# Performance work log

Hardware: AMD Instinct MI355X
Metric: run time of the kernel (lower is better)

## Reference

```python
import jax, jax.numpy as jnp
import numpy as np

EPS = 0.1
MAX_ITER = 100
THRESH = 0.1


def setup_inputs() -> dict:
    key = jax.random.key(0)
    k1, k2, k3, k4 = jax.random.split(key, 4)
    N, P1, P2, D = 4, 1024, 1024, 16
    x = jax.random.normal(k1, (N, P1, D), dtype=jnp.float32)
    y = jax.random.normal(k2, (N, P2, D), dtype=jnp.float32)
    wx = jax.random.uniform(k3, (N, P1), dtype=jnp.float32)
    wy = jax.random.uniform(k4, (N, P2), dtype=jnp.float32)
    # normalize to probability weights (typical usage for empirical measures)
    wx = wx / jnp.sum(wx, axis=-1, keepdims=True)
    wy = wy / jnp.sum(wy, axis=-1, keepdims=True)
    return {"x": x, "y": y, "wx": wx, "wy": wy}


def _cost_matrix(x, y):
    # |x_i - y_j|^1 summed over feature dim -> [N, P1, P2]
    return jnp.sum(jnp.abs(x[:, :, None, :] - y[:, None, :, :]), axis=-1)


def reference(x, y, wx, wy):
    C = _cost_matrix(x, y)                     # [N, P1, P2]
    mu, nu = wx, wy                            # [N, P1], [N, P2]
    log_mu = jnp.log(mu + 1e-8)
    log_nu = jnp.log(nu + 1e-8)

    def M(u, v):
        # (-C_ij + u_i + v_j) / eps
        return (-C + u[:, :, None] + v[:, None, :]) / EPS

    def step(carry, _):
        u, v, done = carry
        u_new = EPS * (log_mu - jax.nn.logsumexp(M(u, v), axis=-1)) + u
        v_new = EPS * (log_nu - jax.nn.logsumexp(M(u_new, v), axis=-2)) + v
        err = jnp.mean(jnp.sum(jnp.abs(u_new - u), axis=-1))
        # emulate torch's early break: freeze u,v once converged
        u_out = jnp.where(done, u, u_new)
        v_out = jnp.where(done, v, v_new)
        done = done | (err < THRESH)
        return (u_out, v_out, done), None

    u0 = jnp.zeros_like(mu)
    v0 = jnp.zeros_like(nu)
    (u, v, _), _ = jax.lax.scan(step, (u0, v0, jnp.array(False)), None, length=MAX_ITER)

    pi = jnp.exp(M(u, v))                      # transport plan [N, P1, P2]
    cost = jnp.sum(pi * C, axis=(-2, -1))      # [N]  (reduction='none')
    return cost, pi, C
```

## Files before the change

### kernel.cpp

```cpp
#include <hip/hip_runtime.h>

static constexpr int   NB      = 4;
static constexpr int   PP      = 1024;
static constexpr int   DD      = 16;
static constexpr float EPSV    = 0.1f;
static constexpr float KE      = 14.42695041f;
static constexpr float KL      = 0.0693147181f;
static constexpr int   MAXIT   = 100;
static constexpr float THRESHV = 0.1f;

static constexpr int NBLK = 256;
static constexpr int NTHR = 512;
static constexpr unsigned DONEG = 1000000u;

__device__ __forceinline__ float fexp2(float v) { return __builtin_amdgcn_exp2f(v); }
__device__ __forceinline__ float flog2(float v) { return __builtin_amdgcn_logf(v); }

static constexpr int    ERR_F_OFF     = 4352;
static constexpr size_t WS_ZERO_BYTES = 4352 * 4;
static constexpr size_t ERR_BYTES    = 512 * 4;

static constexpr int VSNAP_OFF = 131072;

__device__ __forceinline__ float aload(const float* p) {
    return __hip_atomic_load(p, __ATOMIC_RELAXED, __HIP_MEMORY_SCOPE_AGENT);
}
__device__ __forceinline__ void astore(float* p, float v) {
    __hip_atomic_store(p, v, __ATOMIC_RELAXED, __HIP_MEMORY_SCOPE_AGENT);
}
__device__ __forceinline__ unsigned aloadu(const unsigned* p) {
    return __hip_atomic_load(p, __ATOMIC_RELAXED, __HIP_MEMORY_SCOPE_AGENT);
}
__device__ __forceinline__ void astoreu(unsigned* p, unsigned v) {
    __hip_atomic_store(p, v, __ATOMIC_RELAXED, __HIP_MEMORY_SCOPE_AGENT);
}
__device__ __forceinline__ float2 aload2(const float* p) {
    unsigned long long v = __hip_atomic_load((const unsigned long long*)p,
                                             __ATOMIC_RELAXED, __HIP_MEMORY_SCOPE_AGENT);
    union { unsigned long long u; float f[2]; } c; c.u = v;
    return make_float2(c.f[0], c.f[1]);
}
__device__ __forceinline__ void astore2(float* p, float a, float b) {
    union { unsigned long long u; float f[2]; } c; c.f[0] = a; c.f[1] = b;
    __hip_atomic_store((unsigned long long*)p, c.u,
                       __ATOMIC_RELAXED, __HIP_MEMORY_SCOPE_AGENT);
}

__device__ __forceinline__ void gbar_group(unsigned* ws32, int n, int g, unsigned gen) {
    __syncthreads();
    if (threadIdx.x < 64) {
        if (threadIdx.x == 0) astoreu(ws32 + (n * 64 + g) * 16, gen);
        const unsigned* sp = ws32 + (n * 64 + threadIdx.x) * 16;
        while (__ballot(aloadu(sp) >= gen) != ~0ull)
            __builtin_amdgcn_s_sleep(1);
    }
    __syncthreads();
}

__global__ __launch_bounds__(NTHR, 2)
void sinkhorn_kernel(const float* __restrict__ x, const float* __restrict__ y,
                     const float* __restrict__ wx, const float* __restrict__ wy,
                     float* __restrict__ out, float* __restrict__ ws)
{
    __shared__ float rt[16 * PP];
    __shared__ float sbuf[PP];
    __shared__ float cred[8];
    __shared__ int   Ts;

    unsigned* ws32  = (unsigned*)ws;
    unsigned* Tslot = ws32 + 4096;
    unsigned* exitf = ws32 + 4104;
    float*    ews   = ws + ERR_F_OFF;

    float* out_cost = out;
    float* out_pi   = out + NB;
    float* out_C    = out + NB + (size_t)NB * PP * PP;

    const int b   = blockIdx.x;
    const int n   = b >> 6;
    const int g   = b & 63;
    const int i0  = g * 16;
    const int w   = threadIdx.x >> 6;
    const int l   = threadIdx.x & 63;
    const int tid = threadIdx.x;

    float* sc = out_C + (size_t)n * PP * PP;

    float4 xr[2][4];
    #pragma unroll
    for (int rr = 0; rr < 2; ++rr) {
        const float4* xp = (const float4*)(x + ((size_t)n * PP + (i0 + 2 * w + rr)) * DD);
        #pragma unroll
        for (int q = 0; q < 4; ++q) xr[rr][q] = xp[q];
    }
    #pragma unroll 4
    for (int k = 0; k < 16; ++k) {
        int j = l + 64 * k;
        const float4* yp = (const float4*)(y + ((size_t)n * PP + j) * DD);
        float4 y0 = yp[0], y1 = yp[1], y2 = yp[2], y3 = yp[3];
        #pragma unroll
        for (int rr = 0; rr < 2; ++rr) {
            float c = fabsf(xr[rr][0].x - y0.x) + fabsf(xr[rr][0].y - y0.y)
                    + fabsf(xr[rr][0].z - y0.z) + fabsf(xr[rr][0].w - y0.w)
                    + fabsf(xr[rr][1].x - y1.x) + fabsf(xr[rr][1].y - y1.y)
                    + fabsf(xr[rr][1].z - y1.z) + fabsf(xr[rr][1].w - y1.w)
                    + fabsf(xr[rr][2].x - y2.x) + fabsf(xr[rr][2].y - y2.y)
                    + fabsf(xr[rr][2].z - y2.z) + fabsf(xr[rr][2].w - y2.w)
                    + fabsf(xr[rr][3].x - y3.x) + fabsf(xr[rr][3].y - y3.y)
                    + fabsf(xr[rr][3].z - y3.z) + fabsf(xr[rr][3].w - y3.w);
            rt[(2 * w + rr) * PP + j] = c;
        }
    }

    float4 yc[2][4];
    #pragma unroll
    for (int c = 0; c < 2; ++c) {
        const float4* yp = (const float4*)(y + ((size_t)n * PP + (i0 + 2 * w + c)) * DD);
        #pragma unroll
        for (int q = 0; q < 4; ++q) yc[c][q] = yp[q];
    }
    float2 c2[16];
    #pragma unroll 4
    for (int k = 0; k < 16; ++k) {
        const float4* xp = (const float4*)(x + ((size_t)n * PP + (l + 64 * k)) * DD);
        float4 x0 = xp[0], x1 = xp[1], x2 = xp[2], x3 = xp[3];
        float cc[2];
        #pragma unroll
        for (int c = 0; c < 2; ++c) {
            cc[c] = fabsf(x0.x - yc[c][0].x) + fabsf(x0.y - yc[c][0].y)
                  + fabsf(x0.z - yc[c][0].z) + fabsf(x0.w - yc[c][0].w)
                  + fabsf(x1.x - yc[c][1].x) + fabsf(x1.y - yc[c][1].y)
                  + fabsf(x1.z - yc[c][1].z) + fabsf(x1.w - yc[c][1].w)
                  + fabsf(x2.x - yc[c][2].x) + fabsf(x2.y - yc[c][2].y)
                  + fabsf(x2.z - yc[c][2].z) + fabsf(x2.w - yc[c][2].w)
                  + fabsf(x3.x - yc[c][3].x) + fabsf(x3.y - yc[c][3].y)
                  + fabsf(x3.z - yc[c][3].z) + fabsf(x3.w - yc[c][3].w);
        }
        c2[k] = make_float2(cc[0], cc[1]);
    }

    float lmu[2], lnu[2];
    #pragma unroll
    for (int rr = 0; rr < 2; ++rr) {
        lmu[rr] = __logf(wx[n * PP + i0 + 2 * w + rr] + 1e-8f);
        lnu[rr] = __logf(wy[n * PP + i0 + 2 * w + rr] + 1e-8f);
    }

    float uprev0 = 0.f, uprev1 = 0.f;

    #pragma unroll 1
    for (int t = 0; t < MAXIT; ++t) {
        if (t >= 2) {
            unsigned ef = aloadu(exitf + n);
            if (ef != 0u && t >= (int)ef + 1) break;
        }

        if (t == 0) {
            sbuf[2 * tid] = 0.f; sbuf[2 * tid + 1] = 0.f;
        } else {
            float2 vp = aload2(sc + VSNAP_OFF + (size_t)(t - 1) * PP + 2 * tid);
            sbuf[2 * tid] = vp.x; sbuf[2 * tid + 1] = vp.y;
        }
        __syncthreads();

        {
            float4 tt[2][4];
            float m0 = -3.4e38f, m1 = -3.4e38f;
            #pragma unroll
            for (int k = 0; k < 4; ++k) {
                int j = 256 * k + 4 * l;
                float4 v4 = *(const float4*)&sbuf[j];
                float4 ca = *(const float4*)&rt[(2 * w) * PP + j];
                float4 cb = *(const float4*)&rt[(2 * w + 1) * PP + j];
                tt[0][k] = make_float4(v4.x - ca.x, v4.y - ca.y, v4.z - ca.z, v4.w - ca.w);
                tt[1][k] = make_float4(v4.x - cb.x, v4.y - cb.y, v4.z - cb.z, v4.w - cb.w);
                m0 = fmaxf(m0, fmaxf(fmaxf(tt[0][k].x, tt[0][k].y), fmaxf(tt[0][k].z, tt[0][k].w)));
                m1 = fmaxf(m1, fmaxf(fmaxf(tt[1][k].x, tt[1][k].y), fmaxf(tt[1][k].z, tt[1][k].w)));
            }
            #pragma unroll
            for (int off = 32; off >= 1; off >>= 1) {
                m0 = fmaxf(m0, __shfl_xor(m0, off));
                m1 = fmaxf(m1, __shfl_xor(m1, off));
            }
            float s0 = 0.f, s1 = 0.f;
            #pragma unroll
            for (int k = 0; k < 4; ++k) {
                s0 += fexp2((tt[0][k].x - m0) * KE) + fexp2((tt[0][k].y - m0) * KE)
                    + fexp2((tt[0][k].z - m0) * KE) + fexp2((tt[0][k].w - m0) * KE);
                s1 += fexp2((tt[1][k].x - m1) * KE) + fexp2((tt[1][k].y - m1) * KE)
                    + fexp2((tt[1][k].z - m1) * KE) + fexp2((tt[1][k].w - m1) * KE);
            }
            #pragma unroll
            for (int off = 32; off >= 1; off >>= 1) {
                s0 += __shfl_xor(s0, off);
                s1 += __shfl_xor(s1, off);
            }
            float un0 = EPSV * lmu[0] - (m0 + KL * flog2(s0));
            float un1 = EPSV * lmu[1] - (m1 + KL * flog2(s1));
            if (l == 0) astore2(sc + (size_t)t * PP + i0 + 2 * w, un0, un1);
        }

        gbar_group(ws32, n, g, (unsigned)(2 * t + 1));

        {
            float2 up = aload2(sc + (size_t)t * PP + 2 * tid);
            sbuf[2 * tid] = up.x; sbuf[2 * tid + 1] = up.y;
            float we = fabsf(up.x - uprev0) + fabsf(up.y - uprev1);
            uprev0 = up.x; uprev1 = up.y;
            #pragma unroll
            for (int off = 32; off >= 1; off >>= 1) we += __shfl_xor(we, off);
            if (l == 0) cred[w] = we;
        }
        __syncthreads();

        {
            float tt0[16], tt1[16], m0 = -3.4e38f, m1 = -3.4e38f;
            #pragma unroll
            for (int k = 0; k < 16; ++k) {
                float uu = sbuf[l + 64 * k];
                tt0[k] = uu - c2[k].x;
                tt1[k] = uu - c2[k].y;
                m0 = fmaxf(m0, tt0[k]);
                m1 = fmaxf(m1, tt1[k]);
            }
            #pragma unroll
            for (int off = 32; off >= 1; off >>= 1) {
                m0 = fmaxf(m0, __shfl_xor(m0, off));
                m1 = fmaxf(m1, __shfl_xor(m1, off));
            }
            float s0 = 0.f, s1 = 0.f;
            #pragma unroll
            for (int k = 0; k < 16; ++k) {
                s0 += fexp2((tt0[k] - m0) * KE);
                s1 += fexp2((tt1[k] - m1) * KE);
            }
            #pragma unroll
            for (int off = 32; off >= 1; off >>= 1) {
                s0 += __shfl_xor(s0, off);
                s1 += __shfl_xor(s1, off);
            }
            float vn0 = EPSV * lnu[0] - (m0 + KL * flog2(s0));
            float vn1 = EPSV * lnu[1] - (m1 + KL * flog2(s1));
            if (l == 0)
                astore2(sc + VSNAP_OFF + (size_t)t * PP + i0 + 2 * w, vn0, vn1);
        }
        if (g == 0 && tid == 0) {
            float es = cred[0] + cred[1] + cred[2] + cred[3]
                     + cred[4] + cred[5] + cred[6] + cred[7];
            astore(ews + n * 128 + t, es);
        }

        __syncthreads();
        if (tid < 64) {
            if (tid == 0) astoreu(ws32 + (n * 64 + g) * 16, (unsigned)(2 * t + 2));
            if (g == 0) {
                float s1f = aload(ews + 0 * 128 + tid) + aload(ews + 1 * 128 + tid)
                          + aload(ews + 2 * 128 + tid) + aload(ews + 3 * 128 + tid);
                float s2f = aload(ews + 0 * 128 + 64 + tid) + aload(ews + 1 * 128 + 64 + tid)
                          + aload(ews + 2 * 128 + 64 + tid) + aload(ews + 3 * 128 + 64 + tid);
                unsigned long long bb = __ballot(s1f < THRESHV * (float)NB)
                                      | __ballot(s2f < THRESHV * (float)NB);
                if (bb != 0ull && tid == 0 && aloadu(exitf + n) == 0u)
                    astoreu(exitf + n, (unsigned)(t + 1));
            }
            const unsigned* sp = ws32 + (n * 64 + tid) * 16;
            while (__ballot(aloadu(sp) >= (unsigned)(2 * t + 2)) != ~0ull)
                __builtin_amdgcn_s_sleep(1);
        }
        __syncthreads();
    }

    if (g == 0 && tid == 0) astoreu(ws32 + (n * 64) * 16, DONEG);

    if (b == 0 && tid < 64) {
        for (;;) {
            bool ok = (tid >= 4) || (aloadu(ws32 + tid * 64 * 16) >= DONEG);
            if (__ballot(ok) == ~0ull) break;
            __builtin_amdgcn_s_sleep(2);
        }
        float s1f = aload(ews + 0 * 128 + tid) + aload(ews + 1 * 128 + tid)
                  + aload(ews + 2 * 128 + tid) + aload(ews + 3 * 128 + tid);
        float s2f = aload(ews + 0 * 128 + 64 + tid) + aload(ews + 1 * 128 + 64 + tid)
                  + aload(ews + 2 * 128 + 64 + tid) + aload(ews + 3 * 128 + 64 + tid);
        unsigned long long b1 = __ballot(s1f < THRESHV * (float)NB);
        unsigned long long b2 = __ballot(s2f < THRESHV * (float)NB);
        int T = b1 ? (__ffsll((long long)b1) - 1)
                   : (b2 ? 64 + (__ffsll((long long)b2) - 1) : MAXIT - 1);
        if (tid == 0) astoreu(Tslot, (unsigned)(T + 1));
    }
    if (tid == 0) {
        unsigned tv;
        while ((tv = aloadu(Tslot)) == 0u) __builtin_amdgcn_s_sleep(2);
        Ts = (int)tv - 1;
    }
    __syncthreads();
    const int T = Ts;

    float u_loc[2];
    {
        float2 up = aload2(sc + (size_t)T * PP + i0 + 2 * w);
        u_loc[0] = up.x; u_loc[1] = up.y;
        float2 vp = aload2(sc + VSNAP_OFF + (size_t)T * PP + 2 * tid);
        sbuf[2 * tid] = vp.x; sbuf[2 * tid + 1] = vp.y;
    }
    gbar_group(ws32, n, g, DONEG + 1u);

    float cacc = 0.f;
    #pragma unroll
    for (int rr = 0; rr < 2; ++rr) {
        int r = 2 * w + rr;
        int i = i0 + r;
        float un = u_loc[rr];
        #pragma unroll
        for (int k = 0; k < 4; ++k) {
            int j = 256 * k + 4 * l;
            float4 c4 = *(const float4*)&rt[r * PP + j];
            float4 v4 = *(const float4*)&sbuf[j];
            float4 p4;
            p4.x = fexp2((un + v4.x - c4.x) * KE);
            p4.y = fexp2((un + v4.y - c4.y) * KE);
            p4.z = fexp2((un + v4.z - c4.z) * KE);
            p4.w = fexp2((un + v4.w - c4.w) * KE);
            *(float4*)&out_pi[((size_t)n * PP + i) * PP + j] = p4;
            *(float4*)&out_C [((size_t)n * PP + i) * PP + j] = c4;
            cacc += p4.x * c4.x + p4.y * c4.y + p4.z * c4.z + p4.w * c4.w;
        }
    }
    #pragma unroll
    for (int off = 32; off >= 1; off >>= 1) cacc += __shfl_xor(cacc, off);
    if (l == 0) cred[w] = cacc;
    __syncthreads();
    if (tid == 0) {
        float s = 0.f;
        #pragma unroll
        for (int q = 0; q < 8; ++q) s += cred[q];
        atomicAdd(&out_cost[n], s);
    }
}

extern "C" void kernel_launch(void* const* d_in, const int* in_sizes, int n_in,
                              void* d_out, int out_size, void* d_ws, size_t ws_size,
                              hipStream_t stream) {
    const float* x  = (const float*)d_in[0];
    const float* y  = (const float*)d_in[1];
    const float* wx = (const float*)d_in[2];
    const float* wy = (const float*)d_in[3];
    float* out = (float*)d_out;
    float* ws  = (float*)d_ws;

    (void)hipMemsetAsync(d_ws, 0, WS_ZERO_BYTES, stream);
    (void)hipMemsetAsync((char*)d_ws + WS_ZERO_BYTES, 0x7f, ERR_BYTES, stream);
    (void)hipMemsetAsync(d_out, 0, NB * sizeof(float), stream);

    hipLaunchKernelGGL(sinkhorn_kernel, dim3(NBLK), dim3(NTHR), 0, stream,
                       x, y, wx, wy, out, ws);
}
```

Before: 805.4 us.

## Replace per-half-iteration group barriers with tagged dataflow polling on u/v values

Removes the two group-wide barriers per Sinkhorn iteration. Each u/v value is now stored as a 64-bit word carrying the float and a tag, and consumers spin until the tags are nonzero, which gives fine-grained producer-consumer synchronisation. Early-exit detection moves to group 0, which piggybacks an exit bit on its u tags so all blocks can stop on the same iteration. In exchange, the scratch area inside out_C doubles in size and must be zeroed by an extra large memset before every launch, and polling on individual elements adds memory traffic.

```diff
diff --git a/kernel.cpp b/kernel.cpp
--- a/kernel.cpp
+++ b/kernel.cpp
@@ -11,17 +11,20 @@
 
 static constexpr int NBLK = 256;
 static constexpr int NTHR = 512;
-static constexpr unsigned DONEG = 1000000u;
+static constexpr unsigned DONEG   = 1000000u;
+static constexpr unsigned TAG1    = 1u;
+static constexpr unsigned EXITBIT = 2u;
+
+static constexpr int    ERR_F_OFF     = 4352;
+static constexpr size_t WS_ZERO_BYTES = 4352 * 4;
+static constexpr size_t ERR_BYTES     = 512 * 4;
+
+static constexpr int    VOFF = MAXIT * PP;
+static constexpr size_t TAGB = (size_t)2 * MAXIT * PP * 8;
 
 __device__ __forceinline__ float fexp2(float v) { return __builtin_amdgcn_exp2f(v); }
 __device__ __forceinline__ float flog2(float v) { return __builtin_amdgcn_logf(v); }
 
-static constexpr int    ERR_F_OFF     = 4352;
-static constexpr size_t WS_ZERO_BYTES = 4352 * 4;
-static constexpr size_t ERR_BYTES    = 512 * 4;
-
-static constexpr int VSNAP_OFF = 131072;
-
 __device__ __forceinline__ float aload(const float* p) {
     return __hip_atomic_load(p, __ATOMIC_RELAXED, __HIP_MEMORY_SCOPE_AGENT);
 }
@@ -34,16 +37,24 @@
 __device__ __forceinline__ void astoreu(unsigned* p, unsigned v) {
     __hip_atomic_store(p, v, __ATOMIC_RELAXED, __HIP_MEMORY_SCOPE_AGENT);
 }
-__device__ __forceinline__ float2 aload2(const float* p) {
-    unsigned long long v = __hip_atomic_load((const unsigned long long*)p,
-                                             __ATOMIC_RELAXED, __HIP_MEMORY_SCOPE_AGENT);
-    union { unsigned long long u; float f[2]; } c; c.u = v;
-    return make_float2(c.f[0], c.f[1]);
-}
-__device__ __forceinline__ void astore2(float* p, float a, float b) {
-    union { unsigned long long u; float f[2]; } c; c.f[0] = a; c.f[1] = b;
-    __hip_atomic_store((unsigned long long*)p, c.u,
-                       __ATOMIC_RELAXED, __HIP_MEMORY_SCOPE_AGENT);
+__device__ __forceinline__ unsigned long long aload64(const unsigned long long* p) {
+    return __hip_atomic_load(p, __ATOMIC_RELAXED, __HIP_MEMORY_SCOPE_AGENT);
+}
+__device__ __forceinline__ void astore_tag(unsigned long long* p, float v, unsigned tag) {
+    union { unsigned long long u; unsigned w[2]; } c;
+    c.w[0] = __float_as_uint(v); c.w[1] = tag;
+    __hip_atomic_store(p, c.u, __ATOMIC_RELAXED, __HIP_MEMORY_SCOPE_AGENT);
+}
+__device__ __forceinline__ void poll_pair(const unsigned long long* p,
+                                          float& f0, float& f1, unsigned& tags) {
+    unsigned long long a = aload64(p), b = aload64(p + 1);
+    while (((unsigned)(a >> 32) == 0u) | ((unsigned)(b >> 32) == 0u)) {
+        __builtin_amdgcn_s_sleep(1);
+        a = aload64(p); b = aload64(p + 1);
+    }
+    f0 = __uint_as_float((unsigned)a);
+    f1 = __uint_as_float((unsigned)b);
+    tags = (unsigned)((a >> 32) | (b >> 32));
 }
 
 __device__ __forceinline__ void gbar_group(unsigned* ws32, int n, int g, unsigned gen) {
@@ -66,10 +77,11 @@
     __shared__ float sbuf[PP];
     __shared__ float cred[8];
     __shared__ int   Ts;
+    __shared__ int   s_last;
+    __shared__ int   s_exit_known;
 
     unsigned* ws32  = (unsigned*)ws;
     unsigned* Tslot = ws32 + 4096;
-    unsigned* exitf = ws32 + 4104;
     float*    ews   = ws + ERR_F_OFF;
 
     float* out_cost = out;
@@ -84,7 +96,9 @@
     const int l   = threadIdx.x & 63;
     const int tid = threadIdx.x;
 
-    float* sc = out_C + (size_t)n * PP * PP;
+    unsigned long long* tsc = (unsigned long long*)(out_C + (size_t)n * PP * PP);
+
+    if (tid == 0) { s_last = 0; s_exit_known = 0; }
 
     float4 xr[2][4];
     #pragma unroll
@@ -150,16 +164,12 @@
 
     #pragma unroll 1
     for (int t = 0; t < MAXIT; ++t) {
-        if (t >= 2) {
-            unsigned ef = aloadu(exitf + n);
-            if (ef != 0u && t >= (int)ef + 1) break;
-        }
-
         if (t == 0) {
             sbuf[2 * tid] = 0.f; sbuf[2 * tid + 1] = 0.f;
         } else {
-            float2 vp = aload2(sc + VSNAP_OFF + (size_t)(t - 1) * PP + 2 * tid);
-            sbuf[2 * tid] = vp.x; sbuf[2 * tid + 1] = vp.y;
+            float v0, v1; unsigned tg;
+            poll_pair(tsc + VOFF + (size_t)(t - 1) * PP + 2 * tid, v0, v1, tg);
+            sbuf[2 * tid] = v0; sbuf[2 * tid + 1] = v1;
         }
         __syncthreads();
 
@@ -197,21 +207,35 @@
             }
             float un0 = EPSV * lmu[0] - (m0 + KL * flog2(s0));
             float un1 = EPSV * lmu[1] - (m1 + KL * flog2(s1));
-            if (l == 0) astore2(sc + (size_t)t * PP + i0 + 2 * w, un0, un1);
-        }
-
-        gbar_group(ws32, n, g, (unsigned)(2 * t + 1));
+            if (l == 0) {
+                unsigned tg = TAG1 | ((g == 0 && s_exit_known) ? EXITBIT : 0u);
+                astore_tag(tsc + (size_t)t * PP + i0 + 2 * w,     un0, tg);
+                astore_tag(tsc + (size_t)t * PP + i0 + 2 * w + 1, un1, tg);
+            }
+        }
+        __syncthreads();
 
         {
-            float2 up = aload2(sc + (size_t)t * PP + 2 * tid);
-            sbuf[2 * tid] = up.x; sbuf[2 * tid + 1] = up.y;
-            float we = fabsf(up.x - uprev0) + fabsf(up.y - uprev1);
-            uprev0 = up.x; uprev1 = up.y;
+            float ux, uy; unsigned tgs;
+            poll_pair(tsc + (size_t)t * PP + 2 * tid, ux, uy, tgs);
+            sbuf[2 * tid] = ux; sbuf[2 * tid + 1] = uy;
+            if (tgs & EXITBIT) s_last = 1;
+            float we = fabsf(ux - uprev0) + fabsf(uy - uprev1);
+            uprev0 = ux; uprev1 = uy;
             #pragma unroll
             for (int off = 32; off >= 1; off >>= 1) we += __shfl_xor(we, off);
             if (l == 0) cred[w] = we;
         }
         __syncthreads();
+
+        float d1 = 0.f, d2 = 0.f;
+        const bool do_det = (g == 0) && (tid < 64) && (s_exit_known == 0);
+        if (do_det) {
+            d1 = aload(ews + 0 * 128 + tid) + aload(ews + 1 * 128 + tid)
+               + aload(ews + 2 * 128 + tid) + aload(ews + 3 * 128 + tid);
+            d2 = aload(ews + 0 * 128 + 64 + tid) + aload(ews + 1 * 128 + 64 + tid)
+               + aload(ews + 2 * 128 + 64 + tid) + aload(ews + 3 * 128 + 64 + tid);
+        }
 
         {
             float tt0[16], tt1[16], m0 = -3.4e38f, m1 = -3.4e38f;
@@ -241,40 +265,37 @@
             }
             float vn0 = EPSV * lnu[0] - (m0 + KL * flog2(s0));
             float vn1 = EPSV * lnu[1] - (m1 + KL * flog2(s1));
-            if (l == 0)
-                astore2(sc + VSNAP_OFF + (size_t)t * PP + i0 + 2 * w, vn0, vn1);
-        }
+            if (l == 0) {
+                astore_tag(tsc + VOFF + (size_t)t * PP + i0 + 2 * w,     vn0, TAG1);
+                astore_tag(tsc + VOFF + (size_t)t * PP + i0 + 2 * w + 1, vn1, TAG1);
+            }
+        }
+
         if (g == 0 && tid == 0) {
             float es = cred[0] + cred[1] + cred[2] + cred[3]
                      + cred[4] + cred[5] + cred[6] + cred[7];
             astore(ews + n * 128 + t, es);
         }
+        if (do_det) {
+            unsigned long long bb = __ballot(d1 < THRESHV * (float)NB)
+                                  | __ballot(d2 < THRESHV * (float)NB);
+            if (bb != 0ull && tid == 0) s_exit_known = 1;
+        }
 
         __syncthreads();
-        if (tid < 64) {
-            if (tid == 0) astoreu(ws32 + (n * 64 + g) * 16, (unsigned)(2 * t + 2));
-            if (g == 0) {
-                float s1f = aload(ews + 0 * 128 + tid) + aload(ews + 1 * 128 + tid)
-                          + aload(ews + 2 * 128 + tid) + aload(ews + 3 * 128 + tid);
-                float s2f = aload(ews + 0 * 128 + 64 + tid) + aload(ews + 1 * 128 + 64 + tid)
-                          + aload(ews + 2 * 128 + 64 + tid) + aload(ews + 3 * 128 + 64 + tid);
-                unsigned long long bb = __ballot(s1f < THRESHV * (float)NB)
-                                      | __ballot(s2f < THRESHV * (float)NB);
-                if (bb != 0ull && tid == 0 && aloadu(exitf + n) == 0u)
-                    astoreu(exitf + n, (unsigned)(t + 1));
-            }
-            const unsigned* sp = ws32 + (n * 64 + tid) * 16;
-            while (__ballot(aloadu(sp) >= (unsigned)(2 * t + 2)) != ~0ull)
-                __builtin_amdgcn_s_sleep(1);
-        }
-        __syncthreads();
-    }
-
-    if (g == 0 && tid == 0) astoreu(ws32 + (n * 64) * 16, DONEG);
+        if (s_last) break;
+        if (tid == 0) s_last = 0;
+    }
+
+    if (g == 0 && tid == 0)
+        __hip_atomic_store(ws32 + (n * 64) * 16, DONEG,
+                           __ATOMIC_RELEASE, __HIP_MEMORY_SCOPE_AGENT);
 
     if (b == 0 && tid < 64) {
         for (;;) {
-            bool ok = (tid >= 4) || (aloadu(ws32 + tid * 64 * 16) >= DONEG);
+            bool ok = (tid >= 4) ||
+                (__hip_atomic_load(ws32 + tid * 64 * 16,
+                                   __ATOMIC_ACQUIRE, __HIP_MEMORY_SCOPE_AGENT) >= DONEG);
             if (__ballot(ok) == ~0ull) break;
             __builtin_amdgcn_s_sleep(2);
         }
@@ -286,11 +307,15 @@
         unsigned long long b2 = __ballot(s2f < THRESHV * (float)NB);
         int T = b1 ? (__ffsll((long long)b1) - 1)
                    : (b2 ? 64 + (__ffsll((long long)b2) - 1) : MAXIT - 1);
-        if (tid == 0) astoreu(Tslot, (unsigned)(T + 1));
+        if (tid == 0)
+            __hip_atomic_store(Tslot, (unsigned)(T + 1),
+                               __ATOMIC_RELEASE, __HIP_MEMORY_SCOPE_AGENT);
     }
     if (tid == 0) {
         unsigned tv;
-        while ((tv = aloadu(Tslot)) == 0u) __builtin_amdgcn_s_sleep(2);
+        while ((tv = __hip_atomic_load(Tslot, __ATOMIC_ACQUIRE,
+                                       __HIP_MEMORY_SCOPE_AGENT)) == 0u)
+            __builtin_amdgcn_s_sleep(2);
         Ts = (int)tv - 1;
     }
     __syncthreads();
@@ -298,10 +323,11 @@
 
     float u_loc[2];
     {
-        float2 up = aload2(sc + (size_t)T * PP + i0 + 2 * w);
-        u_loc[0] = up.x; u_loc[1] = up.y;
-        float2 vp = aload2(sc + VSNAP_OFF + (size_t)T * PP + 2 * tid);
-        sbuf[2 * tid] = vp.x; sbuf[2 * tid + 1] = vp.y;
+        unsigned tg;
+        poll_pair(tsc + (size_t)T * PP + i0 + 2 * w, u_loc[0], u_loc[1], tg);
+        float v0, v1;
+        poll_pair(tsc + VOFF + (size_t)T * PP + 2 * tid, v0, v1, tg);
+        sbuf[2 * tid] = v0; sbuf[2 * tid + 1] = v1;
     }
     gbar_group(ws32, n, g, DONEG + 1u);
 
@@ -351,6 +377,11 @@
     (void)hipMemsetAsync(d_ws, 0, WS_ZERO_BYTES, stream);
     (void)hipMemsetAsync((char*)d_ws + WS_ZERO_BYTES, 0x7f, ERR_BYTES, stream);
     (void)hipMemsetAsync(d_out, 0, NB * sizeof(float), stream);
+    {
+        size_t out_C_off = ((size_t)NB + (size_t)NB * PP * PP) * sizeof(float);
+        size_t span = (size_t)(NB - 1) * PP * PP * sizeof(float) + TAGB;
+        (void)hipMemsetAsync((char*)d_out + out_C_off, 0, span, stream);
+    }
 
     hipLaunchKernelGGL(sinkhorn_kernel, dim3(NBLK), dim3(NTHR), 0, stream,
                        x, y, wx, wy, out, ws);
```

Measured after the change: 884.8 us. 1.1x slower.

## Double block count to one row per wave across 512 persistent blocks

Applied to the files above, without the earlier changes.

Splits the work across 512 blocks (128 per batch) instead of 256, so each wave handles one row/column instead of two, halving the cost-matrix tile in shared memory and allowing 4 blocks per CU. The grid barrier now polls 128 group flags per batch, two per lane. This spreads the per-iteration logsumexp work over more CUs, at the cost of more participants in every grid-wide barrier and the need for all 512 blocks to be co-resident.

```diff
diff --git a/kernel.cpp b/kernel.cpp
--- a/kernel.cpp
+++ b/kernel.cpp
@@ -9,18 +9,20 @@
 static constexpr int   MAXIT   = 100;
 static constexpr float THRESHV = 0.1f;
 
-static constexpr int NBLK = 256;
+static constexpr int NBLK = 512;
+static constexpr int GPB  = 128;
+static constexpr int RPB  = 8;
 static constexpr int NTHR = 512;
 static constexpr unsigned DONEG = 1000000u;
 
+static constexpr int    ERR_F_OFF     = 8448;
+static constexpr size_t WS_ZERO_BYTES = 8448 * 4;
+static constexpr size_t ERR_BYTES     = 512 * 4;
+
+static constexpr int VSNAP_OFF = 131072;
+
 __device__ __forceinline__ float fexp2(float v) { return __builtin_amdgcn_exp2f(v); }
 __device__ __forceinline__ float flog2(float v) { return __builtin_amdgcn_logf(v); }
-
-static constexpr int    ERR_F_OFF     = 4352;
-static constexpr size_t WS_ZERO_BYTES = 4352 * 4;
-static constexpr size_t ERR_BYTES    = 512 * 4;
-
-static constexpr int VSNAP_OFF = 131072;
 
 __device__ __forceinline__ float aload(const float* p) {
     return __hip_atomic_load(p, __ATOMIC_RELAXED, __HIP_MEMORY_SCOPE_AGENT);
@@ -40,36 +42,32 @@
     union { unsigned long long u; float f[2]; } c; c.u = v;
     return make_float2(c.f[0], c.f[1]);
 }
-__device__ __forceinline__ void astore2(float* p, float a, float b) {
-    union { unsigned long long u; float f[2]; } c; c.f[0] = a; c.f[1] = b;
-    __hip_atomic_store((unsigned long long*)p, c.u,
-                       __ATOMIC_RELAXED, __HIP_MEMORY_SCOPE_AGENT);
-}
 
 __device__ __forceinline__ void gbar_group(unsigned* ws32, int n, int g, unsigned gen) {
     __syncthreads();
     if (threadIdx.x < 64) {
-        if (threadIdx.x == 0) astoreu(ws32 + (n * 64 + g) * 16, gen);
-        const unsigned* sp = ws32 + (n * 64 + threadIdx.x) * 16;
-        while (__ballot(aloadu(sp) >= gen) != ~0ull)
+        if (threadIdx.x == 0) astoreu(ws32 + (n * GPB + g) * 16, gen);
+        const unsigned* sa = ws32 + (n * GPB + 2 * threadIdx.x) * 16;
+        const unsigned* sb = sa + 16;
+        while (__ballot((aloadu(sa) >= gen) & (aloadu(sb) >= gen)) != ~0ull)
             __builtin_amdgcn_s_sleep(1);
     }
     __syncthreads();
 }
 
-__global__ __launch_bounds__(NTHR, 2)
+__global__ __launch_bounds__(NTHR, 4)
 void sinkhorn_kernel(const float* __restrict__ x, const float* __restrict__ y,
                      const float* __restrict__ wx, const float* __restrict__ wy,
                      float* __restrict__ out, float* __restrict__ ws)
 {
-    __shared__ float rt[16 * PP];
+    __shared__ float rt[RPB * PP];
     __shared__ float sbuf[PP];
     __shared__ float cred[8];
     __shared__ int   Ts;
 
     unsigned* ws32  = (unsigned*)ws;
-    unsigned* Tslot = ws32 + 4096;
-    unsigned* exitf = ws32 + 4104;
+    unsigned* Tslot = ws32 + 8192;
+    unsigned* exitf = ws32 + 8200;
     float*    ews   = ws + ERR_F_OFF;
 
     float* out_cost = out;
@@ -77,74 +75,60 @@
     float* out_C    = out + NB + (size_t)NB * PP * PP;
 
     const int b   = blockIdx.x;
-    const int n   = b >> 6;
-    const int g   = b & 63;
-    const int i0  = g * 16;
+    const int n   = b >> 7;
+    const int g   = b & (GPB - 1);
+    const int i0  = g * RPB;
     const int w   = threadIdx.x >> 6;
     const int l   = threadIdx.x & 63;
     const int tid = threadIdx.x;
 
     float* sc = out_C + (size_t)n * PP * PP;
 
-    float4 xr[2][4];
-    #pragma unroll
-    for (int rr = 0; rr < 2; ++rr) {
-        const float4* xp = (const float4*)(x + ((size_t)n * PP + (i0 + 2 * w + rr)) * DD);
+    float4 xr[4];
+    {
+        const float4* xp = (const float4*)(x + ((size_t)n * PP + (i0 + w)) * DD);
         #pragma unroll
-        for (int q = 0; q < 4; ++q) xr[rr][q] = xp[q];
+        for (int q = 0; q < 4; ++q) xr[q] = xp[q];
     }
     #pragma unroll 4
     for (int k = 0; k < 16; ++k) {
         int j = l + 64 * k;
         const float4* yp = (const float4*)(y + ((size_t)n * PP + j) * DD);
         float4 y0 = yp[0], y1 = yp[1], y2 = yp[2], y3 = yp[3];
+        float c = fabsf(xr[0].x - y0.x) + fabsf(xr[0].y - y0.y)
+                + fabsf(xr[0].z - y0.z) + fabsf(xr[0].w - y0.w)
+                + fabsf(xr[1].x - y1.x) + fabsf(xr[1].y - y1.y)
+                + fabsf(xr[1].z - y1.z) + fabsf(xr[1].w - y1.w)
+                + fabsf(xr[2].x - y2.x) + fabsf(xr[2].y - y2.y)
+                + fabsf(xr[2].z - y2.z) + fabsf(xr[2].w - y2.w)
+                + fabsf(xr[3].x - y3.x) + fabsf(xr[3].y - y3.y)
+                + fabsf(xr[3].z - y3.z) + fabsf(xr[3].w - y3.w);
+        rt[w * PP + j] = c;
+    }
+
+    float4 yc[4];
+    {
+        const float4* yp = (const float4*)(y + ((size_t)n * PP + (i0 + w)) * DD);
         #pragma unroll
-        for (int rr = 0; rr < 2; ++rr) {
-            float c = fabsf(xr[rr][0].x - y0.x) + fabsf(xr[rr][0].y - y0.y)
-                    + fabsf(xr[rr][0].z - y0.z) + fabsf(xr[rr][0].w - y0.w)
-                    + fabsf(xr[rr][1].x - y1.x) + fabsf(xr[rr][1].y - y1.y)
-                    + fabsf(xr[rr][1].z - y1.z) + fabsf(xr[rr][1].w - y1.w)
-                    + fabsf(xr[rr][2].x - y2.x) + fabsf(xr[rr][2].y - y2.y)
-                    + fabsf(xr[rr][2].z - y2.z) + fabsf(xr[rr][2].w - y2.w)
-                    + fabsf(xr[rr][3].x - y3.x) + fabsf(xr[rr][3].y - y3.y)
-                    + fabsf(xr[rr][3].z - y3.z) + fabsf(xr[rr][3].w - y3.w);
-            rt[(2 * w + rr) * PP + j] = c;
-        }
-    }
-
-    float4 yc[2][4];
-    #pragma unroll
-    for (int c = 0; c < 2; ++c) {
-        const float4* yp = (const float4*)(y + ((size_t)n * PP + (i0 + 2 * w + c)) * DD);
-        #pragma unroll
-        for (int q = 0; q < 4; ++q) yc[c][q] = yp[q];
-    }
-    float2 c2[16];
+        for (int q = 0; q < 4; ++q) yc[q] = yp[q];
+    }
+    float c2[16];
     #pragma unroll 4
     for (int k = 0; k < 16; ++k) {
         const float4* xp = (const float4*)(x + ((size_t)n * PP + (l + 64 * k)) * DD);
         float4 x0 = xp[0], x1 = xp[1], x2 = xp[2], x3 = xp[3];
-        float cc[2];
-        #pragma unroll
-        for (int c = 0; c < 2; ++c) {
-            cc[c] = fabsf(x0.x - yc[c][0].x) + fabsf(x0.y - yc[c][0].y)
-                  + fabsf(x0.z - yc[c][0].z) + fabsf(x0.w - yc[c][0].w)
-                  + fabsf(x1.x - yc[c][1].x) + fabsf(x1.y - yc[c][1].y)
-                  + fabsf(x1.z - yc[c][1].z) + fabsf(x1.w - yc[c][1].w)
-                  + fabsf(x2.x - yc[c][2].x) + fabsf(x2.y - yc[c][2].y)
-                  + fabsf(x2.z - yc[c][2].z) + fabsf(x2.w - yc[c][2].w)
-                  + fabsf(x3.x - yc[c][3].x) + fabsf(x3.y - yc[c][3].y)
-                  + fabsf(x3.z - yc[c][3].z) + fabsf(x3.w - yc[c][3].w);
-        }
-        c2[k] = make_float2(cc[0], cc[1]);
-    }
-
-    float lmu[2], lnu[2];
-    #pragma unroll
-    for (int rr = 0; rr < 2; ++rr) {
-        lmu[rr] = __logf(wx[n * PP + i0 + 2 * w + rr] + 1e-8f);
-        lnu[rr] = __logf(wy[n * PP + i0 + 2 * w + rr] + 1e-8f);
-    }
+        c2[k] = fabsf(x0.x - yc[0].x) + fabsf(x0.y - yc[0].y)
+              + fabsf(x0.z - yc[0].z) + fabsf(x0.w - yc[0].w)
+              + fabsf(x1.x - yc[1].x) + fabsf(x1.y - yc[1].y)
+              + fabsf(x1.z - yc[1].z) + fabsf(x1.w - yc[1].w)
+              + fabsf(x2.x - yc[2].x) + fabsf(x2.y - yc[2].y)
+              + fabsf(x2.z - yc[2].z) + fabsf(x2.w - yc[2].w)
+              + fabsf(x3.x - yc[3].x) + fabsf(x3.y - yc[3].y)
+              + fabsf(x3.z - yc[3].z) + fabsf(x3.w - yc[3].w);
+    }
+
+    const float lmu = __logf(wx[n * PP + i0 + w] + 1e-8f);
+    const float lnu = __logf(wy[n * PP + i0 + w] + 1e-8f);
 
     float uprev0 = 0.f, uprev1 = 0.f;
 
@@ -164,40 +148,30 @@
         __syncthreads();
 
         {
-            float4 tt[2][4];
-            float m0 = -3.4e38f, m1 = -3.4e38f;
+            float4 tt[4];
+            float m0 = -3.4e38f;
             #pragma unroll
             for (int k = 0; k < 4; ++k) {
                 int j = 256 * k + 4 * l;
                 float4 v4 = *(const float4*)&sbuf[j];
-                float4 ca = *(const float4*)&rt[(2 * w) * PP + j];
-                float4 cb = *(const float4*)&rt[(2 * w + 1) * PP + j];
-                tt[0][k] = make_float4(v4.x - ca.x, v4.y - ca.y, v4.z - ca.z, v4.w - ca.w);
-                tt[1][k] = make_float4(v4.x - cb.x, v4.y - cb.y, v4.z - cb.z, v4.w - cb.w);
-                m0 = fmaxf(m0, fmaxf(fmaxf(tt[0][k].x, tt[0][k].y), fmaxf(tt[0][k].z, tt[0][k].w)));
-                m1 = fmaxf(m1, fmaxf(fmaxf(tt[1][k].x, tt[1][k].y), fmaxf(tt[1][k].z, tt[1][k].w)));
+                float4 ca = *(const float4*)&rt[w * PP + j];
+                tt[k] = make_float4(v4.x - ca.x, v4.y - ca.y, v4.z - ca.z, v4.w - ca.w);
+                m0 = fmaxf(m0, fmaxf(fmaxf(tt[k].x, tt[k].y), fmaxf(tt[k].z, tt[k].w)));
             }
             #pragma unroll
-            for (int off = 32; off >= 1; off >>= 1) {
+            for (int off = 32; off >= 1; off >>= 1)
                 m0 = fmaxf(m0, __shfl_xor(m0, off));
-                m1 = fmaxf(m1, __shfl_xor(m1, off));
+            float s0 = 0.f;
+            #pragma unroll
+            for (int k = 0; k < 4; ++k) {
+                s0 += fexp2((tt[k].x - m0) * KE) + fexp2((tt[k].y - m0) * KE)
+                    + fexp2((tt[k].z - m0) * KE) + fexp2((tt[k].w - m0) * KE);
             }
-            float s0 = 0.f, s1 = 0.f;
-            #pragma unroll
-            for (int k = 0; k < 4; ++k) {
-                s0 += fexp2((tt[0][k].x - m0) * KE) + fexp2((tt[0][k].y - m0) * KE)
-                    + fexp2((tt[0][k].z - m0) * KE) + fexp2((tt[0][k].w - m0) * KE);
-                s1 += fexp2((tt[1][k].x - m1) * KE) + fexp2((tt[1][k].y - m1) * KE)
-                    + fexp2((tt[1][k].z - m1) * KE) + fexp2((tt[1][k].w - m1) * KE);
-            }
-            #pragma unroll
-            for (int off = 32; off >= 1; off >>= 1) {
+            #pragma unroll
+            for (int off = 32; off >= 1; off >>= 1)
                 s0 += __shfl_xor(s0, off);
-                s1 += __shfl_xor(s1, off);
-            }
-            float un0 = EPSV * lmu[0] - (m0 + KL * flog2(s0));
-            float un1 = EPSV * lmu[1] - (m1 + KL * flog2(s1));
-            if (l == 0) astore2(sc + (size_t)t * PP + i0 + 2 * w, un0, un1);
+            float un0 = EPSV * lmu - (m0 + KL * flog2(s0));
+            if (l == 0) astore(sc + (size_t)t * PP + i0 + w, un0);
         }
 
         gbar_group(ws32, n, g, (unsigned)(2 * t + 1));
@@ -214,35 +188,26 @@
         __syncthreads();
 
         {
-            float tt0[16], tt1[16], m0 = -3.4e38f, m1 = -3.4e38f;
+            float tt0[16], m0 = -3.4e38f;
             #pragma unroll
             for (int k = 0; k < 16; ++k) {
                 float uu = sbuf[l + 64 * k];
-                tt0[k] = uu - c2[k].x;
-                tt1[k] = uu - c2[k].y;
+                tt0[k] = uu - c2[k];
                 m0 = fmaxf(m0, tt0[k]);
-                m1 = fmaxf(m1, tt1[k]);
             }
             #pragma unroll
-            for (int off = 32; off >= 1; off >>= 1) {
+            for (int off = 32; off >= 1; off >>= 1)
                 m0 = fmaxf(m0, __shfl_xor(m0, off));
-                m1 = fmaxf(m1, __shfl_xor(m1, off));
-            }
-            float s0 = 0.f, s1 = 0.f;
-            #pragma unroll
-            for (int k = 0; k < 16; ++k) {
+            float s0 = 0.f;
+            #pragma unroll
+            for (int k = 0; k < 16; ++k)
                 s0 += fexp2((tt0[k] - m0) * KE);
-                s1 += fexp2((tt1[k] - m1) * KE);
-            }
-            #pragma unroll
-            for (int off = 32; off >= 1; off >>= 1) {
+            #pragma unroll
+            for (int off = 32; off >= 1; off >>= 1)
                 s0 += __shfl_xor(s0, off);
-                s1 += __shfl_xor(s1, off);
-            }
-            float vn0 = EPSV * lnu[0] - (m0 + KL * flog2(s0));
-            float vn1 = EPSV * lnu[1] - (m1 + KL * flog2(s1));
+            float vn0 = EPSV * lnu - (m0 + KL * flog2(s0));
             if (l == 0)
-                astore2(sc + VSNAP_OFF + (size_t)t * PP + i0 + 2 * w, vn0, vn1);
+                astore(sc + VSNAP_OFF + (size_t)t * PP + i0 + w, vn0);
         }
         if (g == 0 && tid == 0) {
             float es = cred[0] + cred[1] + cred[2] + cred[3]
@@ -252,7 +217,7 @@
 
         __syncthreads();
         if (tid < 64) {
-            if (tid == 0) astoreu(ws32 + (n * 64 + g) * 16, (unsigned)(2 * t + 2));
+            if (tid == 0) astoreu(ws32 + (n * GPB + g) * 16, (unsigned)(2 * t + 2));
             if (g == 0) {
                 float s1f = aload(ews + 0 * 128 + tid) + aload(ews + 1 * 128 + tid)
                           + aload(ews + 2 * 128 + tid) + aload(ews + 3 * 128 + tid);
@@ -263,18 +228,20 @@
                 if (bb != 0ull && tid == 0 && aloadu(exitf + n) == 0u)
                     astoreu(exitf + n, (unsigned)(t + 1));
             }
-            const unsigned* sp = ws32 + (n * 64 + tid) * 16;
-            while (__ballot(aloadu(sp) >= (unsigned)(2 * t + 2)) != ~0ull)
+            const unsigned* sa = ws32 + (n * GPB + 2 * tid) * 16;
+            const unsigned* sb = sa + 16;
+            while (__ballot((aloadu(sa) >= (unsigned)(2 * t + 2)) &
+                            (aloadu(sb) >= (unsigned)(2 * t + 2))) != ~0ull)
                 __builtin_amdgcn_s_sleep(1);
         }
         __syncthreads();
     }
 
-    if (g == 0 && tid == 0) astoreu(ws32 + (n * 64) * 16, DONEG);
+    if (g == 0 && tid == 0) astoreu(ws32 + (n * GPB) * 16, DONEG);
 
     if (b == 0 && tid < 64) {
         for (;;) {
-            bool ok = (tid >= 4) || (aloadu(ws32 + tid * 64 * 16) >= DONEG);
+            bool ok = (tid >= 4) || (aloadu(ws32 + tid * GPB * 16) >= DONEG);
             if (__ballot(ok) == ~0ull) break;
             __builtin_amdgcn_s_sleep(2);
         }
@@ -296,25 +263,22 @@
     __syncthreads();
     const int T = Ts;
 
-    float u_loc[2];
+    float u_loc;
     {
-        float2 up = aload2(sc + (size_t)T * PP + i0 + 2 * w);
-        u_loc[0] = up.x; u_loc[1] = up.y;
+        u_loc = aload(sc + (size_t)T * PP + i0 + w);
         float2 vp = aload2(sc + VSNAP_OFF + (size_t)T * PP + 2 * tid);
         sbuf[2 * tid] = vp.x; sbuf[2 * tid + 1] = vp.y;
     }
     gbar_group(ws32, n, g, DONEG + 1u);
 
     float cacc = 0.f;
-    #pragma unroll
-    for (int rr = 0; rr < 2; ++rr) {
-        int r = 2 * w + rr;
-        int i = i0 + r;
-        float un = u_loc[rr];
+    {
+        int i = i0 + w;
+        float un = u_loc;
         #pragma unroll
         for (int k = 0; k < 4; ++k) {
             int j = 256 * k + 4 * l;
-            float4 c4 = *(const float4*)&rt[r * PP + j];
+            float4 c4 = *(const float4*)&rt[w * PP + j];
             float4 v4 = *(const float4*)&sbuf[j];
             float4 p4;
             p4.x = fexp2((un + v4.x - c4.x) * KE);
```

Result: slower. 873.8 us (+8.5%).

## Replace group barriers with per-producer flag polling and data fetch

Applied to the files above, without the earlier changes.

Drops the full group barrier between the u and v half-steps. Each of the first 64 threads now polls only the flag of its own producer block and, once that flag is set, loads that block's 16-element slice into a padded shared buffer. This lets fetching overlap with late producers and removes the end-of-iteration barrier wait, deferring it until after the loop. The padded layout (stride 17) avoids LDS bank conflicts but gives up float4 LDS reads, and the exit-flag read moves into shared memory via one thread per block.

```diff
diff --git a/kernel.cpp b/kernel.cpp
--- a/kernel.cpp
+++ b/kernel.cpp
@@ -13,14 +13,14 @@
 static constexpr int NTHR = 512;
 static constexpr unsigned DONEG = 1000000u;
 
+static constexpr int    ERR_F_OFF     = 4352;
+static constexpr size_t WS_ZERO_BYTES = 4352 * 4;
+static constexpr size_t ERR_BYTES     = 512 * 4;
+
+static constexpr int VSNAP_OFF = 131072;
+
 __device__ __forceinline__ float fexp2(float v) { return __builtin_amdgcn_exp2f(v); }
 __device__ __forceinline__ float flog2(float v) { return __builtin_amdgcn_logf(v); }
-
-static constexpr int    ERR_F_OFF     = 4352;
-static constexpr size_t WS_ZERO_BYTES = 4352 * 4;
-static constexpr size_t ERR_BYTES    = 512 * 4;
-
-static constexpr int VSNAP_OFF = 131072;
 
 __device__ __forceinline__ float aload(const float* p) {
     return __hip_atomic_load(p, __ATOMIC_RELAXED, __HIP_MEMORY_SCOPE_AGENT);
@@ -44,6 +44,35 @@
     union { unsigned long long u; float f[2]; } c; c.f[0] = a; c.f[1] = b;
     __hip_atomic_store((unsigned long long*)p, c.u,
                        __ATOMIC_RELAXED, __HIP_MEMORY_SCOPE_AGENT);
+}
+
+__device__ __forceinline__ int pidx(int e) { return (e >> 4) * 17 + (e & 15); }
+
+__device__ __forceinline__ void stage_poll(const unsigned* ws32, int n,
+                                           const float* src, unsigned gen,
+                                           float* sbuf2, int tid) {
+    if (tid < 64) {
+        const unsigned* sp = ws32 + (n * 64 + tid) * 16;
+        const float* cp = src + tid * 16;
+        float2 d0, d1, d2, d3, d4, d5, d6, d7;
+        bool got = false;
+        for (;;) {
+            if (!got && aloadu(sp) >= gen) {
+                d0 = aload2(cp + 0);  d1 = aload2(cp + 2);
+                d2 = aload2(cp + 4);  d3 = aload2(cp + 6);
+                d4 = aload2(cp + 8);  d5 = aload2(cp + 10);
+                d6 = aload2(cp + 12); d7 = aload2(cp + 14);
+                got = true;
+            }
+            if (__ballot(got) == ~0ull) break;
+            __builtin_amdgcn_s_sleep(1);
+        }
+        float* dst = sbuf2 + tid * 17;
+        dst[0]  = d0.x; dst[1]  = d0.y; dst[2]  = d1.x; dst[3]  = d1.y;
+        dst[4]  = d2.x; dst[5]  = d2.y; dst[6]  = d3.x; dst[7]  = d3.y;
+        dst[8]  = d4.x; dst[9]  = d4.y; dst[10] = d5.x; dst[11] = d5.y;
+        dst[12] = d6.x; dst[13] = d6.y; dst[14] = d7.x; dst[15] = d7.y;
+    }
 }
 
 __device__ __forceinline__ void gbar_group(unsigned* ws32, int n, int g, unsigned gen) {
@@ -63,9 +92,10 @@
                      float* __restrict__ out, float* __restrict__ ws)
 {
     __shared__ float rt[16 * PP];
-    __shared__ float sbuf[PP];
+    __shared__ float sbuf2[1088];
     __shared__ float cred[8];
     __shared__ int   Ts;
+    __shared__ int   s_ef;
 
     unsigned* ws32  = (unsigned*)ws;
     unsigned* Tslot = ws32 + 4096;
@@ -85,6 +115,8 @@
     const int tid = threadIdx.x;
 
     float* sc = out_C + (size_t)n * PP * PP;
+
+    if (tid == 0) s_ef = 0;
 
     float4 xr[2][4];
     #pragma unroll
@@ -148,18 +180,18 @@
 
     float uprev0 = 0.f, uprev1 = 0.f;
 
+    int last_t = 0;
+
     #pragma unroll 1
     for (int t = 0; t < MAXIT; ++t) {
-        if (t >= 2) {
-            unsigned ef = aloadu(exitf + n);
-            if (ef != 0u && t >= (int)ef + 1) break;
-        }
+        if (t >= 2 && s_ef != 0 && t >= s_ef + 1) break;
+        last_t = t;
 
         if (t == 0) {
-            sbuf[2 * tid] = 0.f; sbuf[2 * tid + 1] = 0.f;
+            sbuf2[pidx(2 * tid)] = 0.f; sbuf2[pidx(2 * tid + 1)] = 0.f;
         } else {
-            float2 vp = aload2(sc + VSNAP_OFF + (size_t)(t - 1) * PP + 2 * tid);
-            sbuf[2 * tid] = vp.x; sbuf[2 * tid + 1] = vp.y;
+            stage_poll(ws32, n, sc + VSNAP_OFF + (size_t)(t - 1) * PP,
+                       (unsigned)(2 * t), sbuf2, tid);
         }
         __syncthreads();
 
@@ -169,11 +201,12 @@
             #pragma unroll
             for (int k = 0; k < 4; ++k) {
                 int j = 256 * k + 4 * l;
-                float4 v4 = *(const float4*)&sbuf[j];
+                float v0 = sbuf2[pidx(j)],     v1 = sbuf2[pidx(j + 1)];
+                float v2 = sbuf2[pidx(j + 2)], v3 = sbuf2[pidx(j + 3)];
                 float4 ca = *(const float4*)&rt[(2 * w) * PP + j];
                 float4 cb = *(const float4*)&rt[(2 * w + 1) * PP + j];
-                tt[0][k] = make_float4(v4.x - ca.x, v4.y - ca.y, v4.z - ca.z, v4.w - ca.w);
-                tt[1][k] = make_float4(v4.x - cb.x, v4.y - cb.y, v4.z - cb.z, v4.w - cb.w);
+                tt[0][k] = make_float4(v0 - ca.x, v1 - ca.y, v2 - ca.z, v3 - ca.w);
+                tt[1][k] = make_float4(v0 - cb.x, v1 - cb.y, v2 - cb.z, v3 - cb.w);
                 m0 = fmaxf(m0, fmaxf(fmaxf(tt[0][k].x, tt[0][k].y), fmaxf(tt[0][k].z, tt[0][k].w)));
                 m1 = fmaxf(m1, fmaxf(fmaxf(tt[1][k].x, tt[1][k].y), fmaxf(tt[1][k].z, tt[1][k].w)));
             }
@@ -199,14 +232,16 @@
             float un1 = EPSV * lmu[1] - (m1 + KL * flog2(s1));
             if (l == 0) astore2(sc + (size_t)t * PP + i0 + 2 * w, un0, un1);
         }
-
-        gbar_group(ws32, n, g, (unsigned)(2 * t + 1));
+        __syncthreads();
+        if (tid == 0) astoreu(ws32 + (n * 64 + g) * 16, (unsigned)(2 * t + 1));
+
+        stage_poll(ws32, n, sc + (size_t)t * PP, (unsigned)(2 * t + 1), sbuf2, tid);
+        __syncthreads();
 
         {
-            float2 up = aload2(sc + (size_t)t * PP + 2 * tid);
-            sbuf[2 * tid] = up.x; sbuf[2 * tid + 1] = up.y;
-            float we = fabsf(up.x - uprev0) + fabsf(up.y - uprev1);
-            uprev0 = up.x; uprev1 = up.y;
+            float up0 = sbuf2[pidx(2 * tid)], up1 = sbuf2[pidx(2 * tid + 1)];
+            float we = fabsf(up0 - uprev0) + fabsf(up1 - uprev1);
+            uprev0 = up0; uprev1 = up1;
             #pragma unroll
             for (int off = 32; off >= 1; off >>= 1) we += __shfl_xor(we, off);
             if (l == 0) cred[w] = we;
@@ -217,7 +252,7 @@
             float tt0[16], tt1[16], m0 = -3.4e38f, m1 = -3.4e38f;
             #pragma unroll
             for (int k = 0; k < 16; ++k) {
-                float uu = sbuf[l + 64 * k];
+                float uu = sbuf2[pidx(l + 64 * k)];
                 tt0[k] = uu - c2[k].x;
                 tt1[k] = uu - c2[k].y;
                 m0 = fmaxf(m0, tt0[k]);
@@ -263,8 +298,16 @@
                 if (bb != 0ull && tid == 0 && aloadu(exitf + n) == 0u)
                     astoreu(exitf + n, (unsigned)(t + 1));
             }
+        }
+        if (tid == 0) s_ef = (int)aloadu(exitf + n);
+        __syncthreads();
+    }
+
+    {
+        const unsigned need = (unsigned)(2 * last_t + 2);
+        if (tid < 64) {
             const unsigned* sp = ws32 + (n * 64 + tid) * 16;
-            while (__ballot(aloadu(sp) >= (unsigned)(2 * t + 2)) != ~0ull)
+            while (__ballot(aloadu(sp) >= need) != ~0ull)
                 __builtin_amdgcn_s_sleep(1);
         }
         __syncthreads();
@@ -301,7 +344,7 @@
         float2 up = aload2(sc + (size_t)T * PP + i0 + 2 * w);
         u_loc[0] = up.x; u_loc[1] = up.y;
         float2 vp = aload2(sc + VSNAP_OFF + (size_t)T * PP + 2 * tid);
-        sbuf[2 * tid] = vp.x; sbuf[2 * tid + 1] = vp.y;
+        sbuf2[pidx(2 * tid)] = vp.x; sbuf2[pidx(2 * tid + 1)] = vp.y;
     }
     gbar_group(ws32, n, g, DONEG + 1u);
 
@@ -315,12 +358,13 @@
         for (int k = 0; k < 4; ++k) {
             int j = 256 * k + 4 * l;
             float4 c4 = *(const float4*)&rt[r * PP + j];
-            float4 v4 = *(const float4*)&sbuf[j];
+            float v0 = sbuf2[pidx(j)],     v1 = sbuf2[pidx(j + 1)];
+            float v2 = sbuf2[pidx(j + 2)], v3 = sbuf2[pidx(j + 3)];
             float4 p4;
-            p4.x = fexp2((un + v4.x - c4.x) * KE);
-            p4.y = fexp2((un + v4.y - c4.y) * KE);
-            p4.z = fexp2((un + v4.z - c4.z) * KE);
-            p4.w = fexp2((un + v4.w - c4.w) * KE);
+            p4.x = fexp2((un + v0 - c4.x) * KE);
+            p4.y = fexp2((un + v1 - c4.y) * KE);
+            p4.z = fexp2((un + v2 - c4.z) * KE);
+            p4.w = fexp2((un + v3 - c4.w) * KE);
             *(float4*)&out_pi[((size_t)n * PP + i) * PP + j] = p4;
             *(float4*)&out_C [((size_t)n * PP + i) * PP + j] = c4;
             cacc += p4.x * c4.x + p4.y * c4.y + p4.z * c4.z + p4.w * c4.w;
```

Result: no change. 797.1 us (-1.0%).
